# Kernel optimization log

Hardware: AMD Instinct MI355X
Metric: run time of the kernel (lower is better)

The kernel has to match this reference:

```python
import jax, jax.numpy as jnp
import numpy as np

B, N, D, H, T, NHOP = 128, 256, 512, 512, 8, 1
NEG = -1e18


def _attn_score(feat, query, v, w):
    # feat: [B, Ns, H], query: [B, Nq, H] -> score [B, Nq, Ns]
    s = jnp.tanh(feat[:, None, :, :] + jnp.matmul(query, w)[:, :, None, :])
    return jnp.einsum('bqnh,h->bqn', s, v)


def _lstm(x, h0, c0, w_ih, w_hh, b_ih, b_hh):
    # x: [B, L, D]; torch nn.LSTM gate order i, f, g, o
    def step(carry, xt):
        h, c = carry
        g = xt @ w_ih.T + h @ w_hh.T + b_ih + b_hh
        i, f, gg, o = jnp.split(g, 4, axis=-1)
        c = jax.nn.sigmoid(f) * c + jax.nn.sigmoid(i) * jnp.tanh(gg)
        h = jax.nn.sigmoid(o) * jnp.tanh(c)
        return (h, c), h
    _, hs = jax.lax.scan(step, (h0, c0), jnp.swapaxes(x, 0, 1))
    return jnp.swapaxes(hs, 0, 1)  # [B, L, H]


def setup_inputs():
    key = jax.random.key(0)
    ks = jax.random.split(key, 17)
    INI = 0.01
    return {
        'attn_mem': jax.random.normal(ks[0], (B, N, D), jnp.float32),
        'lstm_in': jax.random.normal(ks[1], (B, T, D), jnp.float32),
        'mem_sizes': jax.random.randint(ks[2], (B,), 1, N + 1).astype(jnp.int32),
        'init_h': jax.random.uniform(ks[3], (H,), jnp.float32, -INI, INI),
        'init_c': jax.random.uniform(ks[4], (H,), jnp.float32, -INI, INI),
        'init_i': jax.random.uniform(ks[5], (D,), jnp.float32, -0.1, 0.1),
        'stop': jax.random.uniform(ks[6], (D,), jnp.float32, -INI, INI),
        'w_ih': jax.random.normal(ks[7], (4 * H, D), jnp.float32) * 0.02,
        'w_hh': jax.random.normal(ks[8], (4 * H, H), jnp.float32) * 0.02,
        'b_ih': jnp.zeros((4 * H,), jnp.float32),
        'b_hh': jnp.zeros((4 * H,), jnp.float32),
        'attn_wm': jax.random.normal(ks[9], (D, H), jnp.float32) * 0.02,
        'attn_wq': jax.random.normal(ks[10], (H, H), jnp.float32) * 0.02,
        'attn_v': jax.random.uniform(ks[11], (H,), jnp.float32, -INI, INI),
        'hop_wm': jax.random.normal(ks[12], (D, H), jnp.float32) * 0.02,
        'hop_wq': jax.random.normal(ks[13], (H, H), jnp.float32) * 0.02,
        'hop_v': jax.random.uniform(ks[14], (H,), jnp.float32, -INI, INI),
    }


def reference(attn_mem, lstm_in, mem_sizes, init_h, init_c, init_i, stop,
              w_ih, w_hh, b_ih, b_hh, attn_wm, attn_wq, attn_v,
              hop_wm, hop_wq, hop_v):
    b = attn_mem.shape[0]
    # append stop slot: zeros row, scatter-add stop vector at index mem_sizes[i]
    mem = jnp.concatenate([attn_mem, jnp.zeros((b, 1, D), attn_mem.dtype)], axis=1)
    mem = mem.at[jnp.arange(b), mem_sizes].add(stop)
    sizes = mem_sizes + 1
    # _prepare
    attn_feat = mem @ attn_wm   # [B, N+1, H]
    hop_feat = mem @ hop_wm     # [B, N+1, H]
    x = jnp.concatenate([jnp.broadcast_to(init_i, (b, 1, D)), lstm_in], axis=1)
    h0 = jnp.broadcast_to(init_h, (b, H))
    c0 = jnp.broadcast_to(init_c, (b, H))
    query = _lstm(x, h0, c0, w_ih, w_hh, b_ih, b_hh)  # [B, T+1, H]
    # n_hop masked glimpse attention
    mask = jnp.arange(N + 1)[None, :] < sizes[:, None]  # [B, N+1]
    for _ in range(NHOP):
        score = _attn_score(hop_feat, query, hop_v, hop_wq)
        score = jnp.where(mask[:, None, :], score, NEG)
        query = jnp.einsum('bqn,bnh->bqh', jax.nn.softmax(score, axis=-1), hop_feat)
    # final unmasked pointer scores [B, T+1, N+1]
    return _attn_score(attn_feat, query, attn_v, attn_wq)
```

## Files before the change

### kernel.cpp

```cpp
#include <hip/hip_runtime.h>
#include <hip/hip_bf16.h>
#include <math.h>

#define BB   128
#define NPTS 256
#define NP1  257
#define DD   512
#define HH   512
#define G4   2048
#define TP1  9
#define NEGF -1e18f
#define MTOT (BB * NP1)
#define CSC  2.8853900817779268f
#define L2E  1.4426950408889634f
#define NFEAT 2056
#define NGX   144

typedef __attribute__((ext_vector_type(8))) short bf16x8;
typedef __attribute__((ext_vector_type(8))) unsigned short u16x8;
typedef __attribute__((ext_vector_type(4))) float f32x4;

__device__ __forceinline__ float bf2f(unsigned short u)
{
    union { unsigned int i; float f; } x;
    x.i = (unsigned int)u << 16;
    return x.f;
}

__device__ __forceinline__ float sigm(float x)
{
    return __builtin_amdgcn_rcpf(1.0f + __builtin_amdgcn_exp2f(-x * L2E));
}

__device__ __forceinline__ float fast_tanh(float x)
{
    float e = __builtin_amdgcn_exp2f(x * CSC);
    return 1.0f - 2.0f * __builtin_amdgcn_rcpf(e + 1.0f);
}

__device__ __forceinline__ void gl_lds16(const __hip_bfloat16* g, __hip_bfloat16* l)
{
    __builtin_amdgcn_global_load_lds(
        (const __attribute__((address_space(1))) void*)g,
        (__attribute__((address_space(3))) void*)l, 16, 0, 0);
}

__device__ __forceinline__ void stage8(const __hip_bfloat16* const* aptr,
                                       const __hip_bfloat16* const* bptr,
                                       const int* ldsoff,
                                       __hip_bfloat16* A_, __hip_bfloat16* B_, int kt)
{
#pragma unroll
    for (int s = 0; s < 4; ++s) gl_lds16(aptr[s] + kt, A_ + ldsoff[s]);
#pragma unroll
    for (int s = 0; s < 4; ++s) gl_lds16(bptr[s] + kt, B_ + ldsoff[s]);
}

__device__ __forceinline__ void gemm_step(const __hip_bfloat16* A_,
                                          const __hip_bfloat16* B_,
                                          f32x4 (&acc)[4][4],
                                          int wr, int wc, int rA, int kgrp)
{
#pragma unroll
    for (int ks = 0; ks < 2; ++ks) {
        bf16x8 af[4], bfr[4];
#pragma unroll
        for (int fi = 0; fi < 4; ++fi) {
            const int r = wr + fi * 16 + rA;
            const int ch = (ks * 4 + kgrp) ^ (r & 7);
            af[fi] = *(const bf16x8*)(A_ + r * 64 + ch * 8);
        }
#pragma unroll
        for (int fj = 0; fj < 4; ++fj) {
            const int r = wc + fj * 16 + rA;
            const int ch = (ks * 4 + kgrp) ^ (r & 7);
            bfr[fj] = *(const bf16x8*)(B_ + r * 64 + ch * 8);
        }
#pragma unroll
        for (int fi = 0; fi < 4; ++fi)
#pragma unroll
            for (int fj = 0; fj < 4; ++fj)
                acc[fi][fj] = __builtin_amdgcn_mfma_f32_16x16x32_bf16(
                    af[fi], bfr[fj], acc[fi][fj], 0, 0, 0);
    }
}

#define PIPE_ITER(I, NW, Acur, Bcur, Anxt, Bnxt)                              \
    if ((I) < 7) stage8(aptr, bptr, ldsoff, Anxt, Bnxt, ((I) + 1) * 64);      \
    asm volatile("s_waitcnt vmcnt(" NW ")" ::: "memory");                     \
    __builtin_amdgcn_s_barrier();                                             \
    asm volatile("" ::: "memory");                                            \
    gemm_step(Acur, Bcur, acc, wr, wc, rA, kgrp);                             \
    __builtin_amdgcn_s_barrier();                                             \
    asm volatile("" ::: "memory");

#define PIPE_RUN()                                                            \
    stage8(aptr, bptr, ldsoff, As0, Bs0, 0);                                  \
    PIPE_ITER(0, "8", As0, Bs0, As1, Bs1)                                     \
    PIPE_ITER(1, "8", As1, Bs1, As0, Bs0)                                     \
    PIPE_ITER(2, "8", As0, Bs0, As1, Bs1)                                     \
    PIPE_ITER(3, "8", As1, Bs1, As0, Bs0)                                     \
    PIPE_ITER(4, "8", As0, Bs0, As1, Bs1)                                     \
    PIPE_ITER(5, "8", As1, Bs1, As0, Bs0)                                     \
    PIPE_ITER(6, "8", As0, Bs0, As1, Bs1)                                     \
    PIPE_ITER(7, "0", As1, Bs1, As0, Bs0)

__global__ __launch_bounds__(256)
void k_prep(const float* __restrict__ hop_wm, const float* __restrict__ attn_wm,
            const float* __restrict__ hop_wq, const float* __restrict__ attn_wq,
            const float* __restrict__ w_ih, const float* __restrict__ w_hh,
            const float* __restrict__ b_ih, const float* __restrict__ b_hh,
            const float* __restrict__ stop, const float* __restrict__ lstm_in,
            const float* __restrict__ init_i, const float* __restrict__ init_h,
            const float* __restrict__ init_c, const float* __restrict__ Amem,
            __hip_bfloat16* __restrict__ Wt2, __hip_bfloat16* __restrict__ WqtH,
            __hip_bfloat16* __restrict__ WqtA, __hip_bfloat16* __restrict__ wih_bf,
            __hip_bfloat16* __restrict__ whh_bf, float* __restrict__ bsum,
            float* __restrict__ stopm2, __hip_bfloat16* __restrict__ Xbf,
            __hip_bfloat16* __restrict__ h_a, float* __restrict__ cbuf,
            __hip_bfloat16* __restrict__ Abf)
{
    const int x = blockIdx.x, t = threadIdx.x;
    if (x < 256) {
        __shared__ float S[64][69];
        const int mat  = x >> 6;
        const int tile = x & 63;
        const int tr = tile >> 3, tc = tile & 7;
        const float* W = (mat == 0) ? hop_wm : (mat == 1) ? attn_wm
                       : (mat == 2) ? hop_wq : attn_wq;
        __hip_bfloat16* O = (mat == 0) ? Wt2 : (mat == 1) ? (Wt2 + (size_t)512 * DD)
                          : (mat == 2) ? WqtH : WqtA;
        const float scale = (mat == 3) ? 1.0f : CSC;
#pragma unroll
        for (int k = 0; k < 4; ++k) {
            const int r = (t >> 4) + k * 16;
            const int c4 = (t & 15) * 4;
            const float4 v = *(const float4*)(W + (size_t)(tr * 64 + r) * 512 + tc * 64 + c4);
            S[r][c4] = v.x; S[r][c4 + 1] = v.y; S[r][c4 + 2] = v.z; S[r][c4 + 3] = v.w;
        }
        __syncthreads();
        const int oc = tc * 64 + (t >> 2);
        const int j0 = (t & 3) * 16;
        __hip_bfloat16 tmp[16];
#pragma unroll
        for (int j = 0; j < 16; ++j)
            tmp[j] = __float2bfloat16(scale * S[j0 + j][t >> 2]);
        *(bf16x8*)(O + (size_t)oc * 512 + tr * 64 + j0)     = *(bf16x8*)&tmp[0];
        *(bf16x8*)(O + (size_t)oc * 512 + tr * 64 + j0 + 8) = *(bf16x8*)&tmp[8];
    } else if (x == 256) {
#pragma unroll
        for (int i = 0; i < 8; ++i) {
            const int idx = t + 256 * i;
            bsum[idx] = b_ih[idx] + b_hh[idx];
        }
    } else if (x < 273) {
        const int h = (x - 257) * 64 + (t >> 2);
        const int q = t & 3;
        const float* W = (h < 512) ? hop_wm : attn_wm;
        const int col = h & 511;
        float a = 0.f;
        const int k0 = q * 128;
        for (int k = k0; k < k0 + 128; ++k)
            a += stop[k] * W[(size_t)k * HH + col];
        a += __shfl_xor(a, 1);
        a += __shfl_xor(a, 2);
        if (q == 0) stopm2[h] = CSC * a;
    } else if (x < 1425) {
        const int m = x - 273;
        const int bb = m / TP1, tt = m - bb * TP1;
        const float* src = (tt == 0) ? init_i : (lstm_in + (size_t)(bb * 8 + tt - 1) * DD);
        float2 vv = *(const float2*)(src + 2 * t);
        __hip_bfloat16* o = Xbf + (size_t)m * DD + 2 * t;
        o[0] = __float2bfloat16(vv.x);
        o[1] = __float2bfloat16(vv.y);
    } else if (x < 1681) {
        const int idx = (x - 1425) * 256 + t;
        h_a[idx]  = __float2bfloat16(init_h[idx & (HH - 1)]);
        cbuf[idx] = init_c[idx & (HH - 1)];
    } else if (x < 3729) {
        const size_t r = (size_t)(x - 1681) * DD;
        wih_bf[r + t]       = __float2bfloat16(w_ih[r + t]);
        wih_bf[r + t + 256] = __float2bfloat16(w_ih[r + t + 256]);
    } else if (x < 5777) {
        const size_t r = (size_t)(x - 3729) * DD;
        whh_bf[r + t]       = __float2bfloat16(w_hh[r + t]);
        whh_bf[r + t + 256] = __float2bfloat16(w_hh[r + t + 256]);
    } else {
        const int m = (x - 5777) * 2 + (t >> 7);
        const int b = m / NP1;
        const int n = m - b * NP1;
        const int c4 = (t & 127) * 4;
        float4 v = make_float4(0.f, 0.f, 0.f, 0.f);
        if (n < NPTS)
            v = *(const float4*)(Amem + ((size_t)(b * NPTS + n)) * DD + c4);
        __hip_bfloat16* o = Abf + (size_t)m * DD + c4;
        o[0] = __float2bfloat16(v.x);
        o[1] = __float2bfloat16(v.y);
        o[2] = __float2bfloat16(v.z);
        o[3] = __float2bfloat16(v.w);
    }
}

__global__ __launch_bounds__(256)
void k_feat2(const __hip_bfloat16* __restrict__ A,
             const __hip_bfloat16* __restrict__ Bt,
             const float* __restrict__ stopm2,
             const int* __restrict__ msz,
             __hip_bfloat16* __restrict__ E2,
             const __hip_bfloat16* __restrict__ Xbf,
             const __hip_bfloat16* __restrict__ wih,
             const float* __restrict__ bsum,
             float* __restrict__ gatesx)
{
    const int orig = blockIdx.x;
    const bool isg = (orig >= NFEAT);
    int m0, n0;
    const __hip_bfloat16* Ause;
    const __hip_bfloat16* Buse;
    if (!isg) {
        const int wgid = (orig & 7) * 257 + (orig >> 3);
        m0 = (wgid >> 3) * 128;
        n0 = (wgid & 7) * 128;
        Ause = A;  Buse = Bt;
    } else {
        const int idx = orig - NFEAT;
        m0 = (idx >> 4) * 128;
        n0 = (idx & 15) * 128;
        Ause = Xbf;  Buse = wih;
    }

    __shared__ __align__(16) __hip_bfloat16 SM[4][128 * 64];
    __hip_bfloat16* As0 = SM[0];
    __hip_bfloat16* Bs0 = SM[1];
    __hip_bfloat16* As1 = SM[2];
    __hip_bfloat16* Bs1 = SM[3];
    const int tid  = threadIdx.x;
    const int lane = tid & 63;
    const int wid  = tid >> 6;
    const int wr = (wid >> 1) * 64;
    const int wc = (wid & 1) * 64;

    const __hip_bfloat16* aptr[4];
    const __hip_bfloat16* bptr[4];
    int ldsoff[4];
#pragma unroll
    for (int s = 0; s < 4; ++s) {
        const int si = wid * 4 + s;
        const int o = si * 1024 + lane * 16;
        const int row = o >> 7;
        const int chunk = (o >> 4) & 7;
        const int sch = chunk ^ (row & 7);
        aptr[s] = Ause + (size_t)(m0 + row) * DD + sch * 8;
        bptr[s] = Buse + (size_t)(n0 + row) * DD + sch * 8;
        ldsoff[s] = si * 512;
    }

    f32x4 acc[4][4];
#pragma unroll
    for (int i = 0; i < 4; ++i)
#pragma unroll
        for (int j = 0; j < 4; ++j) acc[i][j] = (f32x4){0.f, 0.f, 0.f, 0.f};

    const int rA = lane & 15;
    const int kgrp = lane >> 4;

    PIPE_RUN()

    if (!isg) {
        const bool hopblk = (n0 < 512);
#pragma unroll
        for (int fi = 0; fi < 4; ++fi) {
#pragma unroll
            for (int r = 0; r < 4; ++r) {
                const int m = m0 + wr + fi * 16 + (lane >> 4) * 4 + r;
                const int b = m / NP1;
                const int n = m - b * NP1;
                const int ms = msz[b];
                if (hopblk && n > ms) continue;
                const bool addstop = (n == ms);
#pragma unroll
                for (int fj = 0; fj < 4; ++fj) {
                    const int h = n0 + wc + fj * 16 + (lane & 15);
                    float v = acc[fi][fj][r];
                    if (addstop) v += stopm2[h];
                    E2[(size_t)m * 1024 + h] = __float2bfloat16(__builtin_amdgcn_exp2f(v));
                }
            }
        }
    } else {
#pragma unroll
        for (int fi = 0; fi < 4; ++fi) {
#pragma unroll
            for (int r = 0; r < 4; ++r) {
                const int m = m0 + wr + fi * 16 + (lane >> 4) * 4 + r;
#pragma unroll
                for (int fj = 0; fj < 4; ++fj) {
                    const int h = n0 + wc + fj * 16 + (lane & 15);
                    gatesx[(size_t)m * G4 + h] = acc[fi][fj][r] + bsum[h];
                }
            }
        }
    }
}

__global__ __launch_bounds__(256)
void k_gemm64(const __hip_bfloat16* __restrict__ A,
              const __hip_bfloat16* __restrict__ Bt,
              float* __restrict__ C, int ldc, int expout)
{
    __shared__ __align__(16) __hip_bfloat16 SM[4][64 * 64];
    __hip_bfloat16* As0 = SM[0];
    __hip_bfloat16* Bs0 = SM[1];
    __hip_bfloat16* As1 = SM[2];
    __hip_bfloat16* Bs1 = SM[3];
    const int tid  = threadIdx.x;
    const int lane = tid & 63;
    const int wid  = tid >> 6;
    const int m0 = blockIdx.x * 64;
    const int n0 = blockIdx.y * 64;

    const __hip_bfloat16* aptr[2];
    const __hip_bfloat16* bptr[2];
    int ldsoff[2];
#pragma unroll
    for (int s = 0; s < 2; ++s) {
        const int si = wid * 2 + s;
        const int o = si * 1024 + lane * 16;
        const int row = o >> 7;
        const int chunk = (o >> 4) & 7;
        const int sch = chunk ^ (row & 7);
        aptr[s] = A + (size_t)(m0 + row) * DD + sch * 8;
        bptr[s] = Bt + (size_t)(n0 + row) * DD + sch * 8;
        ldsoff[s] = si * 512;
    }

    f32x4 acc[4];
#pragma unroll
    for (int j = 0; j < 4; ++j) acc[j] = (f32x4){0.f, 0.f, 0.f, 0.f};

    const int rA = lane & 15;
    const int kgrp = lane >> 4;

#define STG64(Abuf, Bbuf, KT)                                                 \
    _Pragma("unroll")                                                         \
    for (int s_ = 0; s_ < 2; ++s_) {                                          \
        gl_lds16(aptr[s_] + (KT), (Abuf) + ldsoff[s_]);                       \
        gl_lds16(bptr[s_] + (KT), (Bbuf) + ldsoff[s_]);                       \
    }
#define G64STEP(A_, B_)                                                       \
    _Pragma("unroll")                                                         \
    for (int ks = 0; ks < 2; ++ks) {                                          \
        const int ra = wid * 16 + rA;                                         \
        const bf16x8 af = *(const bf16x8*)((A_) + ra * 64                     \
                              + (((ks * 4 + kgrp) ^ (ra & 7)) * 8));          \
        _Pragma("unroll")                                                     \
        for (int fj = 0; fj < 4; ++fj) {                                      \
            const int rb = fj * 16 + rA;                                      \
            const bf16x8 bf_ = *(const bf16x8*)((B_) + rb * 64                \
                              + (((ks * 4 + kgrp) ^ (rb & 7)) * 8));          \
            acc[fj] = __builtin_amdgcn_mfma_f32_16x16x32_bf16(                \
                af, bf_, acc[fj], 0, 0, 0);                                   \
        }                                                                     \
    }
#define G64ITER(I, NW, Acur, Bcur, Anxt, Bnxt)                                \
    if ((I) < 7) { STG64(Anxt, Bnxt, ((I) + 1) * 64) }                        \
    asm volatile("s_waitcnt vmcnt(" NW ")" ::: "memory");                     \
    __builtin_amdgcn_s_barrier();                                             \
    asm volatile("" ::: "memory");                                            \
    G64STEP(Acur, Bcur)                                                       \
    __builtin_amdgcn_s_barrier();                                             \
    asm volatile("" ::: "memory");

    STG64(As0, Bs0, 0)
    G64ITER(0, "4", As0, Bs0, As1, Bs1)
    G64ITER(1, "4", As1, Bs1, As0, Bs0)
    G64ITER(2, "4", As0, Bs0, As1, Bs1)
    G64ITER(3, "4", As1, Bs1, As0, Bs0)
    G64ITER(4, "4", As0, Bs0, As1, Bs1)
    G64ITER(5, "4", As1, Bs1, As0, Bs0)
    G64ITER(6, "4", As0, Bs0, As1, Bs1)
    G64ITER(7, "0", As1, Bs1, As0, Bs0)

#pragma unroll
    for (int fj = 0; fj < 4; ++fj) {
#pragma unroll
        for (int r = 0; r < 4; ++r) {
            const int m = m0 + wid * 16 + (lane >> 4) * 4 + r;
            const int h = n0 + fj * 16 + (lane & 15);
            float v = acc[fj][r];
            if (expout) v = __builtin_amdgcn_exp2f(v);
            C[(size_t)m * ldc + h] = v;
        }
    }
}

__global__ __launch_bounds__(256)
void k_lstm2(const __hip_bfloat16* __restrict__ hin,
             const __hip_bfloat16* __restrict__ whh,
             const float* __restrict__ gx,
             float* __restrict__ cbuf,
             __hip_bfloat16* __restrict__ hout,
             __hip_bfloat16* __restrict__ query,
             int t)
{
    __shared__ __align__(16) __hip_bfloat16 As[32 * 512];
    __shared__ __align__(16) __hip_bfloat16 Bs[32 * 512];
    __shared__ float Gs[32][36];
    const int tid  = threadIdx.x;
    const int lane = tid & 63;
    const int wid  = tid >> 6;
    const int m0  = blockIdx.x * 32;
    const int hc0 = blockIdx.y * 8;
    const int wy = wid >> 1, wx = wid & 1;

#pragma unroll
    for (int i = 0; i < 8; ++i) {
        const int o = (i * 256 + tid) * 16;
        const int c = o >> 12;
        const int oc = o & 4095;
        const int row = oc >> 7;
        const int ch = (oc >> 4) & 7;
        const int sch = ch ^ (row & 7);
        gl_lds16(hin + (size_t)(m0 + row) * HH + c * 64 + sch * 8, As + (o >> 1));
    }
#pragma unroll
    for (int i = 0; i < 8; ++i) {
        const int o = (i * 256 + tid) * 16;
        const int c = o >> 12;
        const int oc = o & 4095;
        const int row = oc >> 7;
        const int ch = (oc >> 4) & 7;
        const int sch = ch ^ (row & 7);
        const int brow = (row >> 3) * 512 + hc0 + (row & 7);
        gl_lds16(whh + (size_t)brow * HH + c * 64 + sch * 8, Bs + (o >> 1));
    }
    __syncthreads();

    f32x4 acc = (f32x4){0.f, 0.f, 0.f, 0.f};
    const int rr = lane & 15;
    const int kg = lane >> 4;

#pragma unroll
    for (int ks = 0; ks < 16; ++ks) {
        const int c = ks >> 1, sub = ks & 1;
        const __hip_bfloat16* Ab = As + c * 2048;
        const __hip_bfloat16* Bb = Bs + c * 2048;
        const int ra = wy * 16 + rr;
        const int rb = wx * 16 + rr;
        const bf16x8 af  = *(const bf16x8*)(Ab + ra * 64 + (((sub * 4 + kg) ^ (ra & 7)) * 8));
        const bf16x8 bfr = *(const bf16x8*)(Bb + rb * 64 + (((sub * 4 + kg) ^ (rb & 7)) * 8));
        acc = __builtin_amdgcn_mfma_f32_16x16x32_bf16(af, bfr, acc, 0, 0, 0);
    }

#pragma unroll
    for (int r = 0; r < 4; ++r)
        Gs[wy * 16 + (lane >> 4) * 4 + r][wx * 16 + (lane & 15)] = acc[r];
    __syncthreads();

    const int j = tid & 7;
    const int m = tid >> 3;
    const float* gxr = gx + ((size_t)(m0 + m) * TP1 + t) * G4 + hc0 + j;
    float iv = sigm(Gs[m][j]      + gxr[0]);
    float fv = sigm(Gs[m][8 + j]  + gxr[512]);
    float gv = fast_tanh(Gs[m][16 + j] + gxr[1024]);
    float ov = sigm(Gs[m][24 + j] + gxr[1536]);
    const int ci = (m0 + m) * HH + hc0 + j;
    float cv = fv * cbuf[ci] + iv * gv;
    float hv = ov * fast_tanh(cv);
    cbuf[ci] = cv;
    hout[ci] = __float2bfloat16(hv);
    query[((size_t)(m0 + m) * TP1 + t) * HH + hc0 + j] = __float2bfloat16(hv);
}

__global__ __launch_bounds__(256)
void k_score(const __hip_bfloat16* __restrict__ E2, int efoff,
             const float* __restrict__ Eq,
             const float* __restrict__ v, const int* __restrict__ msz,
             float* __restrict__ score, int masked)
{
    const int wid  = threadIdx.x >> 6;
    const int lane = threadIdx.x & 63;
    const int n = blockIdx.x * 4 + wid;
    const int b = blockIdx.y;
    if (n >= NP1) return;
    float* sp = score + (size_t)b * TP1 * NP1 + n;
    if (masked && n > msz[b]) {
        if (lane == 0)
#pragma unroll
            for (int q = 0; q < TP1; ++q) sp[q * NP1] = NEGF;
        return;
    }
    const u16x8 fu = *(const u16x8*)((const unsigned short*)E2
                                     + ((size_t)b * NP1 + n) * 1024 + efoff + lane * 8);
    float ef[8];
#pragma unroll
    for (int i = 0; i < 8; ++i) ef[i] = bf2f(fu[i]);
    const float4* v4 = (const float4*)v;
    const float4 va = v4[lane * 2], vb = v4[lane * 2 + 1];
    const float vs8 = va.x + va.y + va.z + va.w + vb.x + vb.y + vb.z + vb.w;
    float v2[8] = {2.f*va.x, 2.f*va.y, 2.f*va.z, 2.f*va.w,
                   2.f*vb.x, 2.f*vb.y, 2.f*vb.z, 2.f*vb.w};
    for (int q = 0; q < TP1; ++q) {
        const float4* q4 = (const float4*)(Eq + ((size_t)b * TP1 + q) * HH);
        const float4 qa = q4[lane * 2], qb = q4[lane * 2 + 1];
        float eq[8] = {qa.x, qa.y, qa.z, qa.w, qb.x, qb.y, qb.z, qb.w};
        float acc = 0.f;
#pragma unroll
        for (int i = 0; i < 8; i += 2) {
            const float x0 = fmaf(ef[i],     eq[i],     1.0f);
            const float x1 = fmaf(ef[i + 1], eq[i + 1], 1.0f);
            const float num = fmaf(v2[i], x1, v2[i + 1] * x0);
            acc = fmaf(num, __builtin_amdgcn_rcpf(x0 * x1), acc);
        }
        float s = vs8 - acc;
#pragma unroll
        for (int off = 32; off; off >>= 1) s += __shfl_down(s, off);
        if (lane == 0) sp[q * NP1] = s;
    }
}

__global__ __launch_bounds__(256)
void k_softpv(const float* __restrict__ score, const __hip_bfloat16* __restrict__ E2,
              const int* __restrict__ msz, __hip_bfloat16* __restrict__ outq)
{
    const int b   = blockIdx.x;
    const int ch  = blockIdx.y;
    const int tid = threadIdx.x;
    const int lane = tid & 63, wid = tid >> 6;
    __shared__ float p[TP1][NP1 + 3];
    __shared__ float comb[TP1][256];
    const int nlim = msz[b] + 1;

    const float* sb = score + (size_t)b * TP1 * NP1;
    for (int q = wid; q < TP1; q += 4) {
        const float* srow = sb + q * NP1;
        float mx = NEGF;
        for (int n = lane; n < nlim; n += 64) mx = fmaxf(mx, srow[n]);
#pragma unroll
        for (int off = 32; off; off >>= 1) mx = fmaxf(mx, __shfl_xor(mx, off));
        float sum = 0.f;
        for (int n = lane; n < nlim; n += 64) {
            float e = __builtin_amdgcn_exp2f((srow[n] - mx) * L2E);
            p[q][n] = e;
            sum += e;
        }
#pragma unroll
        for (int off = 32; off; off >>= 1) sum += __shfl_xor(sum, off);
        float inv = 1.f / sum;
        for (int n = lane; n < nlim; n += 64) p[q][n] *= inv;
    }
    __syncthreads();

    const int ng = tid >> 7;
    const int tc = tid & 127;
    const int col = ch * 256 + tc * 2;
    const unsigned short* fb = (const unsigned short*)E2 + (size_t)b * NP1 * 1024 + col;
    float a0[TP1] = {}, a1[TP1] = {};
    for (int n = ng; n < nlim; n += 2) {
        const unsigned int u = *(const unsigned int*)(fb + (size_t)n * 1024);
        const float f0 = __builtin_amdgcn_logf(bf2f((unsigned short)(u & 0xffffu)));
        const float f1 = __builtin_amdgcn_logf(bf2f((unsigned short)(u >> 16)));
#pragma unroll
        for (int q = 0; q < TP1; ++q) {
            const float pq = p[q][n];
            a0[q] += pq * f0;
            a1[q] += pq * f1;
        }
    }
    if (ng == 1) {
#pragma unroll
        for (int q = 0; q < TP1; ++q) {
            comb[q][tc * 2]     = a0[q];
            comb[q][tc * 2 + 1] = a1[q];
        }
    }
    __syncthreads();
    if (ng == 0) {
        __hip_bfloat16* oq = outq + (size_t)(b * TP1) * HH + col;
#pragma unroll
        for (int q = 0; q < TP1; ++q) {
            oq[(size_t)q * HH]     = __float2bfloat16(a0[q] + comb[q][tc * 2]);
            oq[(size_t)q * HH + 1] = __float2bfloat16(a1[q] + comb[q][tc * 2 + 1]);
        }
    }
}

extern "C" void kernel_launch(void* const* d_in, const int* in_sizes, int n_in,
                              void* d_out, int out_size, void* d_ws, size_t ws_size,
                              hipStream_t stream)
{
    const float* attn_mem  = (const float*)d_in[0];
    const float* lstm_in   = (const float*)d_in[1];
    const int*   mem_sizes = (const int*)d_in[2];
    const float* init_h    = (const float*)d_in[3];
    const float* init_c    = (const float*)d_in[4];
    const float* init_i    = (const float*)d_in[5];
    const float* stop      = (const float*)d_in[6];
    const float* w_ih      = (const float*)d_in[7];
    const float* w_hh      = (const float*)d_in[8];
    const float* b_ih      = (const float*)d_in[9];
    const float* b_hh      = (const float*)d_in[10];
    const float* attn_wm   = (const float*)d_in[11];
    const float* attn_wq   = (const float*)d_in[12];
    const float* attn_v    = (const float*)d_in[13];
    const float* hop_wm    = (const float*)d_in[14];
    const float* hop_wq    = (const float*)d_in[15];
    const float* hop_v     = (const float*)d_in[16];
    float* out = (float*)d_out;

    char* w = (char*)d_ws;
    __hip_bfloat16* Abf    = (__hip_bfloat16*)w;  w += (size_t)MTOT * DD * 2;
    __hip_bfloat16* E2     = (__hip_bfloat16*)w;  w += (size_t)MTOT * 1024 * 2;
    __hip_bfloat16* Xbf    = (__hip_bfloat16*)w;  w += (size_t)BB * TP1 * DD * 2;
    __hip_bfloat16* Wt2    = (__hip_bfloat16*)w;  w += (size_t)1024 * DD * 2;
    __hip_bfloat16* WqtH   = (__hip_bfloat16*)w;  w += (size_t)HH * HH * 2;
    __hip_bfloat16* WqtA   = (__hip_bfloat16*)w;  w += (size_t)HH * HH * 2;
    __hip_bfloat16* wih_bf = (__hip_bfloat16*)w;  w += (size_t)G4 * DD * 2;
    __hip_bfloat16* whh_bf = (__hip_bfloat16*)w;  w += (size_t)G4 * HH * 2;
    __hip_bfloat16* h_a    = (__hip_bfloat16*)w;  w += (size_t)BB * HH * 2;
    __hip_bfloat16* h_b    = (__hip_bfloat16*)w;  w += (size_t)BB * HH * 2;
    __hip_bfloat16* query  = (__hip_bfloat16*)w;  w += (size_t)BB * TP1 * HH * 2;
    __hip_bfloat16* query2 = (__hip_bfloat16*)w;  w += (size_t)BB * TP1 * HH * 2;
    float* gatesx  = (float*)w;  w += (size_t)BB * TP1 * G4 * 4;
    float* eq      = (float*)w;  w += (size_t)BB * TP1 * HH * 4;
    float* score   = (float*)w;  w += (size_t)BB * TP1 * NP1 * 4;
    float* cbuf    = (float*)w;  w += (size_t)BB * HH * 4;
    float* stopm2  = (float*)w;  w += 1024 * 4;
    float* bsum    = (float*)w;  w += G4 * 4;

    k_prep<<<dim3(22225), dim3(256), 0, stream>>>(
        hop_wm, attn_wm, hop_wq, attn_wq, w_ih, w_hh, b_ih, b_hh,
        stop, lstm_in, init_i, init_h, init_c, attn_mem,
        Wt2, WqtH, WqtA, wih_bf, whh_bf, bsum, stopm2, Xbf, h_a, cbuf, Abf);

    k_feat2<<<dim3(NFEAT + NGX), dim3(256), 0, stream>>>(
        Abf, Wt2, stopm2, mem_sizes, E2, Xbf, wih_bf, bsum, gatesx);

    for (int t = 0; t < TP1; ++t) {
        const __hip_bfloat16* hin = (t & 1) ? h_b : h_a;
        __hip_bfloat16*      hout = (t & 1) ? h_a : h_b;
        k_lstm2<<<dim3(4, 64), dim3(256), 0, stream>>>(hin, whh_bf, gatesx, cbuf, hout, query, t);
    }

    k_gemm64<<<dim3(18, 8), dim3(256), 0, stream>>>(query, WqtH, eq, HH, 1);
    k_score<<<dim3(65, 128), dim3(256), 0, stream>>>(E2, 0, eq, hop_v, mem_sizes, score, 1);
    k_softpv<<<dim3(128, 2), dim3(256), 0, stream>>>(score, E2, mem_sizes, query2);

    k_gemm64<<<dim3(18, 8), dim3(256), 0, stream>>>(query2, WqtA, eq, HH, 1);
    k_score<<<dim3(65, 128), dim3(256), 0, stream>>>(E2, 512, eq, attn_v, mem_sizes, out, 0);
}
```

Before: 224.6 us.

## Raise wave priority around MFMA loops, split softmax-PV over more blocks, skip masked writes

Wraps the MFMA inner loops of the GEMM, gemm64 and LSTM kernels in s_setprio so compute waves get issue priority over loading waves. The softmax-PV kernel now gives each thread one column instead of two and launches twice as many column chunks, adding parallelism for the batch-sized grid. The masked score kernel no longer writes NEG for masked positions, since softpv reads only up to the mask limit. It also unrolls the query loop in k_score. Dropping the NEG writes leaves those score entries uninitialised, which is safe only because the hop scores are consumed solely by softpv.

```diff
diff --git a/kernel.cpp b/kernel.cpp
--- a/kernel.cpp
+++ b/kernel.cpp
@@ -90,7 +90,9 @@
     asm volatile("s_waitcnt vmcnt(" NW ")" ::: "memory");                     \
     __builtin_amdgcn_s_barrier();                                             \
     asm volatile("" ::: "memory");                                            \
+    __builtin_amdgcn_s_setprio(1);                                            \
     gemm_step(Acur, Bcur, acc, wr, wc, rA, kgrp);                             \
+    __builtin_amdgcn_s_setprio(0);                                            \
     __builtin_amdgcn_s_barrier();                                             \
     asm volatile("" ::: "memory");
 
@@ -367,7 +369,9 @@
     asm volatile("s_waitcnt vmcnt(" NW ")" ::: "memory");                     \
     __builtin_amdgcn_s_barrier();                                             \
     asm volatile("" ::: "memory");                                            \
+    __builtin_amdgcn_s_setprio(1);                                            \
     G64STEP(Acur, Bcur)                                                       \
+    __builtin_amdgcn_s_setprio(0);                                            \
     __builtin_amdgcn_s_barrier();                                             \
     asm volatile("" ::: "memory");
 
@@ -440,6 +444,7 @@
     const int rr = lane & 15;
     const int kg = lane >> 4;
 
+    __builtin_amdgcn_s_setprio(1);
 #pragma unroll
     for (int ks = 0; ks < 16; ++ks) {
         const int c = ks >> 1, sub = ks & 1;
@@ -451,6 +456,7 @@
         const bf16x8 bfr = *(const bf16x8*)(Bb + rb * 64 + (((sub * 4 + kg) ^ (rb & 7)) * 8));
         acc = __builtin_amdgcn_mfma_f32_16x16x32_bf16(af, bfr, acc, 0, 0, 0);
     }
+    __builtin_amdgcn_s_setprio(0);
 
 #pragma unroll
     for (int r = 0; r < 4; ++r)
@@ -483,13 +489,8 @@
     const int n = blockIdx.x * 4 + wid;
     const int b = blockIdx.y;
     if (n >= NP1) return;
+    if (masked && n > msz[b]) return;
     float* sp = score + (size_t)b * TP1 * NP1 + n;
-    if (masked && n > msz[b]) {
-        if (lane == 0)
-#pragma unroll
-            for (int q = 0; q < TP1; ++q) sp[q * NP1] = NEGF;
-        return;
-    }
     const u16x8 fu = *(const u16x8*)((const unsigned short*)E2
                                      + ((size_t)b * NP1 + n) * 1024 + efoff + lane * 8);
     float ef[8];
@@ -500,6 +501,7 @@
     const float vs8 = va.x + va.y + va.z + va.w + vb.x + vb.y + vb.z + vb.w;
     float v2[8] = {2.f*va.x, 2.f*va.y, 2.f*va.z, 2.f*va.w,
                    2.f*vb.x, 2.f*vb.y, 2.f*vb.z, 2.f*vb.w};
+#pragma unroll
     for (int q = 0; q < TP1; ++q) {
         const float4* q4 = (const float4*)(Eq + ((size_t)b * TP1 + q) * HH);
         const float4 qa = q4[lane * 2], qb = q4[lane * 2 + 1];
@@ -528,7 +530,7 @@
     const int tid = threadIdx.x;
     const int lane = tid & 63, wid = tid >> 6;
     __shared__ float p[TP1][NP1 + 3];
-    __shared__ float comb[TP1][256];
+    __shared__ float comb[TP1][128];
     const int nlim = msz[b] + 1;
 
     const float* sb = score + (size_t)b * TP1 * NP1;
@@ -553,35 +555,24 @@
 
     const int ng = tid >> 7;
     const int tc = tid & 127;
-    const int col = ch * 256 + tc * 2;
+    const int col = ch * 128 + tc;
     const unsigned short* fb = (const unsigned short*)E2 + (size_t)b * NP1 * 1024 + col;
-    float a0[TP1] = {}, a1[TP1] = {};
+    float a[TP1] = {};
     for (int n = ng; n < nlim; n += 2) {
-        const unsigned int u = *(const unsigned int*)(fb + (size_t)n * 1024);
-        const float f0 = __builtin_amdgcn_logf(bf2f((unsigned short)(u & 0xffffu)));
-        const float f1 = __builtin_amdgcn_logf(bf2f((unsigned short)(u >> 16)));
-#pragma unroll
-        for (int q = 0; q < TP1; ++q) {
-            const float pq = p[q][n];
-            a0[q] += pq * f0;
-            a1[q] += pq * f1;
-        }
+        const float f = __builtin_amdgcn_logf(bf2f(fb[(size_t)n * 1024]));
+#pragma unroll
+        for (int q = 0; q < TP1; ++q) a[q] += p[q][n] * f;
     }
     if (ng == 1) {
 #pragma unroll
-        for (int q = 0; q < TP1; ++q) {
-            comb[q][tc * 2]     = a0[q];
-            comb[q][tc * 2 + 1] = a1[q];
-        }
+        for (int q = 0; q < TP1; ++q) comb[q][tc] = a[q];
     }
     __syncthreads();
     if (ng == 0) {
         __hip_bfloat16* oq = outq + (size_t)(b * TP1) * HH + col;
 #pragma unroll
-        for (int q = 0; q < TP1; ++q) {
-            oq[(size_t)q * HH]     = __float2bfloat16(a0[q] + comb[q][tc * 2]);
-            oq[(size_t)q * HH + 1] = __float2bfloat16(a1[q] + comb[q][tc * 2 + 1]);
-        }
+        for (int q = 0; q < TP1; ++q)
+            oq[(size_t)q * HH] = __float2bfloat16(a[q] + comb[q][tc]);
     }
 }
 
@@ -644,7 +635,7 @@
 
     k_gemm64<<<dim3(18, 8), dim3(256), 0, stream>>>(query, WqtH, eq, HH, 1);
     k_score<<<dim3(65, 128), dim3(256), 0, stream>>>(E2, 0, eq, hop_v, mem_sizes, score, 1);
-    k_softpv<<<dim3(128, 2), dim3(256), 0, stream>>>(score, E2, mem_sizes, query2);
+    k_softpv<<<dim3(128, 4), dim3(256), 0, stream>>>(score, E2, mem_sizes, query2);
 
     k_gemm64<<<dim3(18, 8), dim3(256), 0, stream>>>(query2, WqtA, eq, HH, 1);
     k_score<<<dim3(65, 128), dim3(256), 0, stream>>>(E2, 512, eq, attn_v, mem_sizes, out, 0);
```

Measured after the change: 225.9 us. About the same (+0.6%).
